# Optimization experiments

Hardware: AMD Instinct MI355X
Metric: run time of the kernel (lower is better)

The kernel has to match this reference:

```python
import jax, jax.numpy as jnp
import numpy as np

B, SA, SB, D, H, DH = 1, 2048, 512, 3072, 24, 128
S = SA + SB
EPS = 1e-6


def _rms_norm(x, w):
    # RMSNorm over last dim (head_dim)
    return x * jax.lax.rsqrt(jnp.mean(x * x, axis=-1, keepdims=True) + EPS) * w


def _make_rope(s, dh):
    # Flux-style rotation matrices: [1,1,S,dh//2,2,2]
    pos = jnp.arange(s, dtype=jnp.float32)
    inv_freq = 1.0 / (10000.0 ** (jnp.arange(0, dh, 2, dtype=jnp.float32) / dh))
    theta = pos[:, None] * inv_freq[None, :]  # [S, dh//2]
    cos, sin = jnp.cos(theta), jnp.sin(theta)
    row0 = jnp.stack([cos, -sin], axis=-1)
    row1 = jnp.stack([sin, cos], axis=-1)
    f = jnp.stack([row0, row1], axis=-2)  # [S, dh//2, 2, 2]
    return f[None, None]


def setup_inputs() -> dict:
    key = jax.random.key(0)
    ks = jax.random.split(key, 12)
    sc = 0.02
    return {
        "hidden_states_a": jax.random.normal(ks[0], (B, SA, D), jnp.float32),
        "hidden_states_b": jax.random.normal(ks[1], (B, SB, D), jnp.float32),
        "image_rotary_emb": _make_rope(S, DH),
        "a_qkv_w": jax.random.normal(ks[2], (3 * D, D), jnp.float32) * sc,
        "a_qkv_b": jnp.zeros((3 * D,), jnp.float32),
        "b_qkv_w": jax.random.normal(ks[3], (3 * D, D), jnp.float32) * sc,
        "b_qkv_b": jnp.zeros((3 * D,), jnp.float32),
        "norm_q_a_w": jnp.ones((DH,), jnp.float32),
        "norm_k_a_w": jnp.ones((DH,), jnp.float32),
        "norm_q_b_w": jnp.ones((DH,), jnp.float32),
        "norm_k_b_w": jnp.ones((DH,), jnp.float32),
        "a_out_w": jax.random.normal(ks[4], (D, D), jnp.float32) * sc,
        "a_out_b": jnp.zeros((D,), jnp.float32),
        "b_out_w": jax.random.normal(ks[5], (D, D), jnp.float32) * sc,
        "b_out_b": jnp.zeros((D,), jnp.float32),
    }


def _apply_rope(x, freqs):
    # x: [B,H,S,DH]; freqs: [1,1,S,DH//2,2,2]
    x_ = x.reshape(*x.shape[:-1], -1, 1, 2)
    out = freqs[..., 0] * x_[..., 0] + freqs[..., 1] * x_[..., 1]  # [B,H,S,DH//2,2]
    return out.reshape(x.shape)


def _qkv(x, w, b):
    bsz, s, _ = x.shape
    qkv = (jnp.einsum('bsd,ed->bse', x, w) + b)
    qkv = qkv.reshape(bsz, s, 3 * H, DH).transpose(0, 2, 1, 3)  # [B,3H,S,DH]
    return jnp.split(qkv, 3, axis=1)


def reference(hidden_states_a, hidden_states_b, image_rotary_emb,
              a_qkv_w, a_qkv_b, b_qkv_w, b_qkv_b,
              norm_q_a_w, norm_k_a_w, norm_q_b_w, norm_k_b_w,
              a_out_w, a_out_b, b_out_w, b_out_b):
    q_a, k_a, v_a = _qkv(hidden_states_a, a_qkv_w, a_qkv_b)
    q_a = _rms_norm(q_a, norm_q_a_w)
    k_a = _rms_norm(k_a, norm_k_a_w)

    q_b, k_b, v_b = _qkv(hidden_states_b, b_qkv_w, b_qkv_b)
    q_b = _rms_norm(q_b, norm_q_b_w)
    k_b = _rms_norm(k_b, norm_k_b_w)

    # text stream first, then image stream
    q = jnp.concatenate([q_b, q_a], axis=2)
    k = jnp.concatenate([k_b, k_a], axis=2)
    v = jnp.concatenate([v_b, v_a], axis=2)

    q = _apply_rope(q, image_rotary_emb)
    k = _apply_rope(k, image_rotary_emb)

    scale = 1.0 / jnp.sqrt(jnp.float32(DH))
    scores = jnp.einsum('bhqd,bhkd->bhqk', q, k) * scale
    attn = jax.nn.softmax(scores, axis=-1)
    o = jnp.einsum('bhqk,bhkd->bhqd', attn, v)  # [B,H,S,DH]
    o = o.transpose(0, 2, 1, 3).reshape(B, S, H * DH)

    out_b, out_a = o[:, :SB], o[:, SB:]
    out_a = jnp.einsum('bsd,ed->bse', out_a, a_out_w) + a_out_b
    out_b = jnp.einsum('bsd,ed->bse', out_b, b_out_w) + b_out_b
    return out_a, out_b
```

## Files before the change

kernel.cpp:

```cpp
#include <hip/hip_runtime.h>
#include <cstdint>
#include <math.h>

typedef unsigned short u16;
typedef __bf16 bf16x8 __attribute__((ext_vector_type(8)));
typedef float f32x4 __attribute__((ext_vector_type(4)));
typedef unsigned int u32x4 __attribute__((ext_vector_type(4)));

#define NH 24
#define DHEAD 128
#define SEQ 2560
#define SEQB 512
#define DMODEL 3072
#define NQKV 9216
#define QSCALE (0.08838834764831845f * 1.4426950408889634f)

__device__ __forceinline__ float bf2f(u16 b) {
  unsigned u = ((unsigned)b) << 16;
  return __builtin_bit_cast(float, u);
}
__device__ __forceinline__ u16 f2bf(float f) {
  unsigned u = __builtin_bit_cast(unsigned, f);
  u += 0x7fffu + ((u >> 16) & 1u);
  return (u16)(u >> 16);
}
__device__ __forceinline__ unsigned pack2(float a, float b) {
  return (unsigned)f2bf(a) | ((unsigned)f2bf(b) << 16);
}

__global__ __launch_bounds__(256) void detect_dtype(const u16* __restrict__ x, int* __restrict__ flag) {
  __shared__ int cnt;
  if (threadIdx.x == 0) cnt = 0;
  __syncthreads();
  int local = 0;
  for (int i = threadIdx.x; i < 262144; i += 256) {
    if ((x[i] & 0x7F80u) == 0x7F80u) local++;
  }
  atomicAdd(&cnt, local);
  __syncthreads();
  if (threadIdx.x == 0) *flag = (cnt > 0) ? 1 : 0;
}

__global__ __launch_bounds__(256) void ingest(const void* __restrict__ src, u16* __restrict__ dst,
                                              int n, const int* __restrict__ flag) {
  const bool f32 = (*flag) != 0;
  int idx = (blockIdx.x * 256 + threadIdx.x) * 8;
  if (idx + 8 <= n) {
    if (f32) {
      const float* s = (const float*)src;
      float4 v0 = *(const float4*)(s + idx);
      float4 v1 = *(const float4*)(s + idx + 4);
      u16 t[8] = {f2bf(v0.x), f2bf(v0.y), f2bf(v0.z), f2bf(v0.w),
                  f2bf(v1.x), f2bf(v1.y), f2bf(v1.z), f2bf(v1.w)};
      *(u32x4*)(dst + idx) = *(u32x4*)t;
    } else {
      *(u32x4*)(dst + idx) = *(const u32x4*)((const u16*)src + idx);
    }
  } else if (idx < n) {
    for (int j = idx; j < n; ++j)
      dst[j] = f32 ? f2bf(((const float*)src)[j]) : ((const u16*)src)[j];
  }
}

__global__ __launch_bounds__(256) void gemm_bt(
    const u16* __restrict__ X, const u16* __restrict__ Wt, const void* __restrict__ bias,
    void* __restrict__ out0, void* __restrict__ out1, void* __restrict__ out2,
    int M, int N, int K, const int* __restrict__ flag, int ext_out, int orow0) {
  __shared__ __align__(16) u16 Asub[128 * 32];
  __shared__ __align__(16) u16 Bsub[128 * 32];
  const int tid = threadIdx.x;
  const int wv = tid >> 6, lane = tid & 63;
  const int lhi = lane >> 4, llo = lane & 15;
  const int n0 = blockIdx.x * 128, m0 = blockIdx.y * 128;
  const int wrow = wv >> 1, wcol = wv & 1;
  f32x4 acc[4][4] = {};
  for (int k0 = 0; k0 < K; k0 += 32) {
    u32x4 areg[2], breg[2];
#pragma unroll
    for (int is = 0; is < 2; ++is) {
      int chunk = is * 256 + tid;
      int row = chunk >> 2, kc = (chunk & 3) << 3;
      areg[is] = *(const u32x4*)(X + (size_t)(m0 + row) * K + k0 + kc);
      breg[is] = *(const u32x4*)(Wt + (size_t)(n0 + row) * K + k0 + kc);
    }
    __syncthreads();
#pragma unroll
    for (int is = 0; is < 2; ++is) {
      int chunk = is * 256 + tid;
      *(u32x4*)&Asub[chunk * 8] = areg[is];
      *(u32x4*)&Bsub[chunk * 8] = breg[is];
    }
    __syncthreads();
    bf16x8 af[4], bfr[4];
#pragma unroll
    for (int t = 0; t < 4; ++t) {
      af[t] = *(const bf16x8*)&Asub[(wrow * 64 + t * 16 + llo) * 32 + lhi * 8];
      bfr[t] = *(const bf16x8*)&Bsub[(wcol * 64 + t * 16 + llo) * 32 + lhi * 8];
    }
#pragma unroll
    for (int i = 0; i < 4; ++i)
#pragma unroll
      for (int j = 0; j < 4; ++j)
        acc[i][j] = __builtin_amdgcn_mfma_f32_16x16x32_bf16(af[i], bfr[j], acc[i][j], 0, 0, 0);
  }
  const bool f32 = (*flag) != 0;
  const int seg = n0 / DMODEL;
  void* ob = seg == 0 ? out0 : (seg == 1 ? out1 : out2);
  const int ocol0 = n0 - seg * DMODEL;
#pragma unroll
  for (int i = 0; i < 4; ++i) {
    int row = m0 + wrow * 64 + i * 16 + lhi * 4;
#pragma unroll
    for (int j = 0; j < 4; ++j) {
      int colin = wcol * 64 + j * 16 + llo;
      float b = f32 ? ((const float*)bias)[n0 + colin] : bf2f(((const u16*)bias)[n0 + colin]);
#pragma unroll
      for (int r = 0; r < 4; ++r) {
        float v = acc[i][j][r] + b;
        size_t off = (size_t)(orow0 + row + r) * DMODEL + ocol0 + colin;
        if (ext_out && f32) ((float*)ob)[off] = v;
        else ((u16*)ob)[off] = f2bf(v);
      }
    }
  }
}

__global__ __launch_bounds__(64) void normrope(
    u16* __restrict__ Qraw, u16* __restrict__ Kraw, const void* __restrict__ rope,
    const void* __restrict__ nqa, const void* __restrict__ nka,
    const void* __restrict__ nqb, const void* __restrict__ nkb,
    const int* __restrict__ flag) {
  const bool f32 = (*flag) != 0;
  int bid = blockIdx.x;
  int which = bid & 1;
  int h = (bid >> 1) % NH;
  int s = bid / (NH * 2);
  int lane = threadIdx.x;
  u16* ptr = (which ? Kraw : Qraw) + (size_t)s * DMODEL + h * DHEAD + lane * 2;
  unsigned xv = *(const unsigned*)ptr;
  float x0 = bf2f((u16)(xv & 0xffff)), x1 = bf2f((u16)(xv >> 16));
  float ss = x0 * x0 + x1 * x1;
#pragma unroll
  for (int m = 1; m < 64; m <<= 1) ss += __shfl_xor(ss, m, 64);
  float rn = rsqrtf(ss * (1.0f / 128.0f) + 1e-6f);
  const void* wn = which ? (s < SEQB ? nkb : nka) : (s < SEQB ? nqb : nqa);
  float w0, w1;
  if (f32) {
    w0 = ((const float*)wn)[lane * 2];
    w1 = ((const float*)wn)[lane * 2 + 1];
  } else {
    unsigned wv2 = *(const unsigned*)((const u16*)wn + lane * 2);
    w0 = bf2f((u16)(wv2 & 0xffff));
    w1 = bf2f((u16)(wv2 >> 16));
  }
  float y0 = x0 * rn * w0;
  float y1 = x1 * rn * w1;
  float c, sn;
  if (f32) {
    const float* rp = (const float*)rope + ((size_t)s * 64 + lane) * 4;
    float4 rv = *(const float4*)rp;
    c = rv.x;
    sn = rv.z;
  } else {
    const u16* rp = (const u16*)rope + ((size_t)s * 64 + lane) * 4;
    uint2 rv = *(const uint2*)rp;
    c = bf2f((u16)(rv.x & 0xffff));
    sn = bf2f((u16)(rv.y & 0xffff));
  }
  float o0 = c * y0 - sn * y1;
  float o1 = sn * y0 + c * y1;
  if (!which) { o0 *= QSCALE; o1 *= QSCALE; }
  *(unsigned*)ptr = pack2(o0, o1);
}

__global__ __launch_bounds__(256) void build_vt(const u16* __restrict__ Vraw, u16* __restrict__ Vt) {
  __shared__ u16 tile[64][66];
  int h = blockIdx.x, st = blockIdx.y, dt = blockIdx.z;
  int s0 = st * 64, d0 = dt * 64;
  int t = threadIdx.x;
  int sl = t >> 5, dp = (t & 31) << 1;
#pragma unroll
  for (int it = 0; it < 8; ++it) {
    int srow = sl + it * 8;
    unsigned v = *(const unsigned*)(Vraw + (size_t)(s0 + srow) * DMODEL + h * DHEAD + d0 + dp);
    tile[srow][dp] = (u16)(v & 0xffff);
    tile[srow][dp + 1] = (u16)(v >> 16);
  }
  __syncthreads();
  int dl = t >> 5, sp = (t & 31) << 1;
#pragma unroll
  for (int it = 0; it < 8; ++it) {
    int drow = dl + it * 8;
    unsigned v = (unsigned)tile[sp][drow] | ((unsigned)tile[sp + 1][drow] << 16);
    *(unsigned*)(Vt + ((size_t)h * DHEAD + d0 + drow) * SEQ + s0 + sp) = v;
  }
}

#define KSTRIDE 136
#define PSTRIDE 40
__global__ __launch_bounds__(256) void attn(
    const u16* __restrict__ Q, const u16* __restrict__ Kd, const u16* __restrict__ Vt,
    u16* __restrict__ O) {
  __shared__ __align__(16) u16 Klds[32 * KSTRIDE];
  __shared__ __align__(16) u16 Vtlds[128 * 32];
  __shared__ __align__(16) u16 Plds[4][16 * PSTRIDE];
  const int q0 = blockIdx.x * 64;
  const int h = blockIdx.y;
  const int tid = threadIdx.x, wv = tid >> 6, lane = tid & 63;
  const int lhi = lane >> 4, llo = lane & 15;
  bf16x8 qf[4];
  const u16* qbase = Q + (size_t)(q0 + wv * 16 + llo) * DMODEL + h * DHEAD + lhi * 8;
#pragma unroll
  for (int f = 0; f < 4; ++f) qf[f] = *(const bf16x8*)(qbase + f * 32);
  float m_[4], l_[4];
  f32x4 oacc[8] = {};
#pragma unroll
  for (int r = 0; r < 4; ++r) { m_[r] = -1e30f; l_[r] = 0.f; }
  for (int kb = 0; kb < SEQ; kb += 32) {
    u32x4 kvv[2], vvv[2];
#pragma unroll
    for (int is = 0; is < 2; ++is) {
      int chunk = is * 256 + tid;
      kvv[is] = *(const u32x4*)(Kd + (size_t)(kb + (chunk >> 4)) * DMODEL + h * DHEAD + ((chunk & 15) << 3));
      vvv[is] = *(const u32x4*)(Vt + ((size_t)h * DHEAD + (chunk >> 2)) * SEQ + kb + ((chunk & 3) << 3));
    }
    __syncthreads();
#pragma unroll
    for (int is = 0; is < 2; ++is) {
      int chunk = is * 256 + tid;
      int krow = chunk >> 4, kslot = chunk & 15;
      *(u32x4*)&Klds[krow * KSTRIDE + kslot * 8] = kvv[is];
      *(u32x4*)&Vtlds[chunk * 8] = vvv[is];
    }
    __syncthreads();
    f32x4 sc[2];
#pragma unroll
    for (int ct = 0; ct < 2; ++ct) {
      f32x4 a = {};
#pragma unroll
      for (int f = 0; f < 4; ++f) {
        bf16x8 kf = *(const bf16x8*)&Klds[(ct * 16 + llo) * KSTRIDE + f * 32 + lhi * 8];
        a = __builtin_amdgcn_mfma_f32_16x16x32_bf16(qf[f], kf, a, 0, 0, 0);
      }
      sc[ct] = a;
    }
    float mnew[4], alpha[4];
#pragma unroll
    for (int r = 0; r < 4; ++r) {
      float mx = fmaxf(sc[0][r], sc[1][r]);
#pragma unroll
      for (int t = 1; t < 16; t <<= 1) mx = fmaxf(mx, __shfl_xor(mx, t, 64));
      mnew[r] = fmaxf(m_[r], mx);
      alpha[r] = exp2f(m_[r] - mnew[r]);
      m_[r] = mnew[r];
    }
    float p[2][4];
#pragma unroll
    for (int ct = 0; ct < 2; ++ct)
#pragma unroll
      for (int r = 0; r < 4; ++r) p[ct][r] = exp2f(sc[ct][r] - mnew[r]);
#pragma unroll
    for (int r = 0; r < 4; ++r) {
      float s = p[0][r] + p[1][r];
#pragma unroll
      for (int t = 1; t < 16; t <<= 1) s += __shfl_xor(s, t, 64);
      l_[r] = l_[r] * alpha[r] + s;
    }
#pragma unroll
    for (int dt = 0; dt < 8; ++dt)
#pragma unroll
      for (int r = 0; r < 4; ++r) oacc[dt][r] *= alpha[r];
    u16* pw = &Plds[wv][0];
#pragma unroll
    for (int ct = 0; ct < 2; ++ct)
#pragma unroll
      for (int r = 0; r < 4; ++r) pw[(lhi * 4 + r) * PSTRIDE + ct * 16 + llo] = f2bf(p[ct][r]);
    bf16x8 pf = *(const bf16x8*)&Plds[wv][llo * PSTRIDE + lhi * 8];
#pragma unroll
    for (int dt = 0; dt < 8; ++dt) {
      bf16x8 vf = *(const bf16x8*)&Vtlds[(dt * 16 + llo) * 32 + lhi * 8];
      oacc[dt] = __builtin_amdgcn_mfma_f32_16x16x32_bf16(pf, vf, oacc[dt], 0, 0, 0);
    }
  }
  float inv[4];
#pragma unroll
  for (int r = 0; r < 4; ++r) inv[r] = 1.0f / l_[r];
#pragma unroll
  for (int dt = 0; dt < 8; ++dt)
#pragma unroll
    for (int r = 0; r < 4; ++r) {
      int row = q0 + wv * 16 + lhi * 4 + r;
      int col = h * DHEAD + dt * 16 + llo;
      O[(size_t)row * DMODEL + col] = f2bf(oacc[dt][r] * inv[r]);
    }
}

extern "C" void kernel_launch(void* const* d_in, const int* in_sizes, int n_in,
                              void* d_out, int out_size, void* d_ws, size_t ws_size,
                              hipStream_t stream) {
  const void* hsa = d_in[0];
  const void* hsb = d_in[1];
  const void* rope = d_in[2];
  const void* aqw = d_in[3];
  const void* aqb = d_in[4];
  const void* bqw = d_in[5];
  const void* bqb = d_in[6];
  const void* nqa = d_in[7];
  const void* nka = d_in[8];
  const void* nqb = d_in[9];
  const void* nkb = d_in[10];
  const void* aow = d_in[11];
  const void* aob = d_in[12];
  const void* bow = d_in[13];
  const void* bob = d_in[14];

  const size_t SEG = (size_t)SEQ * DMODEL;
  u16* Wp = (u16*)d_ws;
  int* flag = (int*)Wp;
  u16* hsac = Wp + 16;
  u16* hsbc = hsac + (size_t)2048 * DMODEL;
  u16* aqwc = hsbc + (size_t)SEQB * DMODEL;
  u16* bqwc = aqwc + (size_t)NQKV * DMODEL;
  u16* Qraw = bqwc + (size_t)NQKV * DMODEL;
  u16* Kraw = Qraw + SEG;
  u16* Vraw = Kraw + SEG;
  u16* Vt = hsac;
  u16* aowc = aqwc;
  u16* bowc = aqwc + (size_t)DMODEL * DMODEL;
  u16* Ob = Vraw;

  detect_dtype<<<1, 256, 0, stream>>>((const u16*)hsa, flag);

  const int n_hsa = 2048 * DMODEL, n_hsb = SEQB * DMODEL;
  const int n_qkvw = NQKV * DMODEL, n_ow = DMODEL * DMODEL;
  ingest<<<(n_hsa / 8 + 255) / 256, 256, 0, stream>>>(hsa, hsac, n_hsa, flag);
  ingest<<<(n_hsb / 8 + 255) / 256, 256, 0, stream>>>(hsb, hsbc, n_hsb, flag);
  ingest<<<(n_qkvw / 8 + 255) / 256, 256, 0, stream>>>(aqw, aqwc, n_qkvw, flag);
  ingest<<<(n_qkvw / 8 + 255) / 256, 256, 0, stream>>>(bqw, bqwc, n_qkvw, flag);

  gemm_bt<<<dim3(NQKV / 128, 2048 / 128), 256, 0, stream>>>(
      hsac, aqwc, aqb,
      Qraw + (size_t)SEQB * DMODEL, Kraw + (size_t)SEQB * DMODEL, Vraw + (size_t)SEQB * DMODEL,
      2048, NQKV, DMODEL, flag, 0, 0);
  gemm_bt<<<dim3(NQKV / 128, SEQB / 128), 256, 0, stream>>>(
      hsbc, bqwc, bqb, Qraw, Kraw, Vraw, SEQB, NQKV, DMODEL, flag, 0, 0);

  ingest<<<(n_ow / 8 + 255) / 256, 256, 0, stream>>>(aow, aowc, n_ow, flag);
  ingest<<<(n_ow / 8 + 255) / 256, 256, 0, stream>>>(bow, bowc, n_ow, flag);

  normrope<<<dim3(SEQ * NH * 2), 64, 0, stream>>>(Qraw, Kraw, rope, nqa, nka, nqb, nkb, flag);
  build_vt<<<dim3(NH, SEQ / 64, DHEAD / 64), 256, 0, stream>>>(Vraw, Vt);
  attn<<<dim3(SEQ / 64, NH), 256, 0, stream>>>(Qraw, Kraw, Vt, Ob);

  gemm_bt<<<dim3(DMODEL / 128, 2048 / 128), 256, 0, stream>>>(
      Ob + (size_t)SEQB * DMODEL, aowc, aob, d_out, d_out, d_out,
      2048, DMODEL, DMODEL, flag, 1, 0);
  gemm_bt<<<dim3(DMODEL / 128, SEQB / 128), 256, 0, stream>>>(
      Ob, bowc, bob, d_out, d_out, d_out, SEQB, DMODEL, DMODEL, flag, 1, 2048);
}
```

Measured before the change: 1.393 ms.

## Double KV tile to 64, prefetch next tile, lazy softmax rescale

The attention kernel now processes 64-key tiles instead of 32, with padded LDS strides for the V and P tiles. Global loads for the next tile are issued right after the LDS store barrier so they overlap compute. The online softmax skips the cross-lane max and rescale unless some row's tile max exceeds the running max by more than 8 (log2 units). Row sums are kept per lane and reduced only once at the end. This cuts shuffle and rescale work and hides load latency, at the cost of more registers and LDS and a bounded risk of bf16 precision loss in P.

After: 1.269 ms. 1.1x faster.

```diff
diff --git a/kernel.cpp b/kernel.cpp
--- a/kernel.cpp
+++ b/kernel.cpp
@@ -196,13 +196,15 @@
   }
 }
 
+#define KVB 64
 #define KSTRIDE 136
-#define PSTRIDE 40
+#define VSTRIDE 72
+#define PSTRIDE 72
 __global__ __launch_bounds__(256) void attn(
     const u16* __restrict__ Q, const u16* __restrict__ Kd, const u16* __restrict__ Vt,
     u16* __restrict__ O) {
-  __shared__ __align__(16) u16 Klds[32 * KSTRIDE];
-  __shared__ __align__(16) u16 Vtlds[128 * 32];
+  __shared__ __align__(16) u16 Klds[KVB * KSTRIDE];
+  __shared__ __align__(16) u16 Vtlds[DHEAD * VSTRIDE];
   __shared__ __align__(16) u16 Plds[4][16 * PSTRIDE];
   const int q0 = blockIdx.x * 64;
   const int h = blockIdx.y;
@@ -212,30 +214,42 @@
   const u16* qbase = Q + (size_t)(q0 + wv * 16 + llo) * DMODEL + h * DHEAD + lhi * 8;
 #pragma unroll
   for (int f = 0; f < 4; ++f) qf[f] = *(const bf16x8*)(qbase + f * 32);
-  float m_[4], l_[4];
+  float m_[4], lp[4];
   f32x4 oacc[8] = {};
 #pragma unroll
-  for (int r = 0; r < 4; ++r) { m_[r] = -1e30f; l_[r] = 0.f; }
-  for (int kb = 0; kb < SEQ; kb += 32) {
-    u32x4 kvv[2], vvv[2];
-#pragma unroll
-    for (int is = 0; is < 2; ++is) {
-      int chunk = is * 256 + tid;
-      kvv[is] = *(const u32x4*)(Kd + (size_t)(kb + (chunk >> 4)) * DMODEL + h * DHEAD + ((chunk & 15) << 3));
-      vvv[is] = *(const u32x4*)(Vt + ((size_t)h * DHEAD + (chunk >> 2)) * SEQ + kb + ((chunk & 3) << 3));
-    }
+  for (int r = 0; r < 4; ++r) { m_[r] = -1e30f; lp[r] = 0.f; }
+
+  u32x4 kvv[4], vvv[4];
+  {
+#pragma unroll
+    for (int is = 0; is < 4; ++is) {
+      int c = is * 256 + tid;
+      kvv[is] = *(const u32x4*)(Kd + (size_t)(c >> 4) * DMODEL + h * DHEAD + ((c & 15) << 3));
+      vvv[is] = *(const u32x4*)(Vt + ((size_t)h * DHEAD + (c >> 3)) * SEQ + ((c & 7) << 3));
+    }
+  }
+
+  for (int kb = 0; kb < SEQ; kb += KVB) {
     __syncthreads();
 #pragma unroll
-    for (int is = 0; is < 2; ++is) {
-      int chunk = is * 256 + tid;
-      int krow = chunk >> 4, kslot = chunk & 15;
-      *(u32x4*)&Klds[krow * KSTRIDE + kslot * 8] = kvv[is];
-      *(u32x4*)&Vtlds[chunk * 8] = vvv[is];
+    for (int is = 0; is < 4; ++is) {
+      int c = is * 256 + tid;
+      *(u32x4*)&Klds[(c >> 4) * KSTRIDE + ((c & 15) << 3)] = kvv[is];
+      *(u32x4*)&Vtlds[(c >> 3) * VSTRIDE + ((c & 7) << 3)] = vvv[is];
     }
     __syncthreads();
-    f32x4 sc[2];
-#pragma unroll
-    for (int ct = 0; ct < 2; ++ct) {
+    if (kb + KVB < SEQ) {
+      int kb2 = kb + KVB;
+#pragma unroll
+      for (int is = 0; is < 4; ++is) {
+        int c = is * 256 + tid;
+        kvv[is] = *(const u32x4*)(Kd + (size_t)(kb2 + (c >> 4)) * DMODEL + h * DHEAD + ((c & 15) << 3));
+        vvv[is] = *(const u32x4*)(Vt + ((size_t)h * DHEAD + (c >> 3)) * SEQ + kb2 + ((c & 7) << 3));
+      }
+    }
+    f32x4 sc[4];
+#pragma unroll
+    for (int ct = 0; ct < 4; ++ct) {
       f32x4 a = {};
 #pragma unroll
       for (int f = 0; f < 4; ++f) {
@@ -244,47 +258,57 @@
       }
       sc[ct] = a;
     }
-    float mnew[4], alpha[4];
-#pragma unroll
-    for (int r = 0; r < 4; ++r) {
-      float mx = fmaxf(sc[0][r], sc[1][r]);
-#pragma unroll
-      for (int t = 1; t < 16; t <<= 1) mx = fmaxf(mx, __shfl_xor(mx, t, 64));
-      mnew[r] = fmaxf(m_[r], mx);
-      alpha[r] = exp2f(m_[r] - mnew[r]);
-      m_[r] = mnew[r];
-    }
-    float p[2][4];
-#pragma unroll
-    for (int ct = 0; ct < 2; ++ct)
-#pragma unroll
-      for (int r = 0; r < 4; ++r) p[ct][r] = exp2f(sc[ct][r] - mnew[r]);
-#pragma unroll
-    for (int r = 0; r < 4; ++r) {
-      float s = p[0][r] + p[1][r];
-#pragma unroll
-      for (int t = 1; t < 16; t <<= 1) s += __shfl_xor(s, t, 64);
-      l_[r] = l_[r] * alpha[r] + s;
-    }
-#pragma unroll
-    for (int dt = 0; dt < 8; ++dt)
-#pragma unroll
-      for (int r = 0; r < 4; ++r) oacc[dt][r] *= alpha[r];
+    float lmax[4];
+#pragma unroll
+    for (int r = 0; r < 4; ++r)
+      lmax[r] = fmaxf(fmaxf(sc[0][r], sc[1][r]), fmaxf(sc[2][r], sc[3][r]));
+    int ok = (lmax[0] <= m_[0] + 8.f) & (lmax[1] <= m_[1] + 8.f) &
+             (lmax[2] <= m_[2] + 8.f) & (lmax[3] <= m_[3] + 8.f);
+    if (!__all(ok)) {
+#pragma unroll
+      for (int r = 0; r < 4; ++r) {
+        float mx = lmax[r];
+#pragma unroll
+        for (int t = 1; t < 16; t <<= 1) mx = fmaxf(mx, __shfl_xor(mx, t, 64));
+        float mnew = fmaxf(m_[r], mx);
+        float alpha = exp2f(m_[r] - mnew);
+        m_[r] = mnew;
+        lp[r] *= alpha;
+#pragma unroll
+        for (int dt = 0; dt < 8; ++dt) oacc[dt][r] *= alpha;
+      }
+    }
+    float p[4][4];
+#pragma unroll
+    for (int ct = 0; ct < 4; ++ct)
+#pragma unroll
+      for (int r = 0; r < 4; ++r) p[ct][r] = exp2f(sc[ct][r] - m_[r]);
+#pragma unroll
+    for (int r = 0; r < 4; ++r)
+      lp[r] += (p[0][r] + p[1][r]) + (p[2][r] + p[3][r]);
     u16* pw = &Plds[wv][0];
 #pragma unroll
-    for (int ct = 0; ct < 2; ++ct)
+    for (int ct = 0; ct < 4; ++ct)
 #pragma unroll
       for (int r = 0; r < 4; ++r) pw[(lhi * 4 + r) * PSTRIDE + ct * 16 + llo] = f2bf(p[ct][r]);
-    bf16x8 pf = *(const bf16x8*)&Plds[wv][llo * PSTRIDE + lhi * 8];
+    bf16x8 pf0 = *(const bf16x8*)&Plds[wv][llo * PSTRIDE + lhi * 8];
+    bf16x8 pf1 = *(const bf16x8*)&Plds[wv][llo * PSTRIDE + 32 + lhi * 8];
 #pragma unroll
     for (int dt = 0; dt < 8; ++dt) {
-      bf16x8 vf = *(const bf16x8*)&Vtlds[(dt * 16 + llo) * 32 + lhi * 8];
-      oacc[dt] = __builtin_amdgcn_mfma_f32_16x16x32_bf16(pf, vf, oacc[dt], 0, 0, 0);
+      bf16x8 vf0 = *(const bf16x8*)&Vtlds[(dt * 16 + llo) * VSTRIDE + lhi * 8];
+      oacc[dt] = __builtin_amdgcn_mfma_f32_16x16x32_bf16(pf0, vf0, oacc[dt], 0, 0, 0);
+      bf16x8 vf1 = *(const bf16x8*)&Vtlds[(dt * 16 + llo) * VSTRIDE + 32 + lhi * 8];
+      oacc[dt] = __builtin_amdgcn_mfma_f32_16x16x32_bf16(pf1, vf1, oacc[dt], 0, 0, 0);
     }
   }
   float inv[4];
 #pragma unroll
-  for (int r = 0; r < 4; ++r) inv[r] = 1.0f / l_[r];
+  for (int r = 0; r < 4; ++r) {
+    float s = lp[r];
+#pragma unroll
+    for (int t = 1; t < 16; t <<= 1) s += __shfl_xor(s, t, 64);
+    inv[r] = 1.0f / s;
+  }
 #pragma unroll
   for (int dt = 0; dt < 8; ++dt)
 #pragma unroll
```
